# Kernel optimization log

Hardware: AMD Instinct MI355X
Metric: run time of the kernel (lower is better)

The kernel has to match this reference:

```python
import jax, jax.numpy as jnp
import numpy as np

E = 512
H = 8
DH = E // H
LN_EPS = 1e-5


def setup_inputs() -> dict:
    key = jax.random.key(0)
    ks = jax.random.split(key, 8)
    s = 1.0 / np.sqrt(E)
    return {
        "query": jax.random.normal(ks[0], (2, 2048, E), jnp.float32),
        "key_value": jax.random.normal(ks[1], (2, 4096, E), jnp.float32),
        "Wq": jax.random.normal(ks[2], (E, E), jnp.float32) * s,
        "bq": jnp.zeros((E,), jnp.float32),
        "Wk": jax.random.normal(ks[3], (E, E), jnp.float32) * s,
        "bk": jnp.zeros((E,), jnp.float32),
        "Wv": jax.random.normal(ks[4], (E, E), jnp.float32) * s,
        "bv": jnp.zeros((E,), jnp.float32),
        "Wo": jax.random.normal(ks[5], (E, E), jnp.float32) * s,
        "bo": jnp.zeros((E,), jnp.float32),
        "ln_gamma": jnp.ones((E,), jnp.float32),
        "ln_beta": jnp.zeros((E,), jnp.float32),
    }


def reference(query, key_value, Wq, bq, Wk, bk, Wv, bv, Wo, bo, ln_gamma, ln_beta):
    B, Lq, _ = query.shape
    Lk = key_value.shape[1]
    # Projections (torch Linear: x @ W.T + b)
    q = (query @ Wq.T + bq).reshape(B, Lq, H, DH)
    k = (key_value @ Wk.T + bk).reshape(B, Lk, H, DH)
    v = (key_value @ Wv.T + bv).reshape(B, Lk, H, DH)
    scale = 1.0 / np.sqrt(DH).astype(np.float32)
    scores = jnp.einsum("bqhd,bkhd->bhqk", q, k) * scale  # [B,H,Lq,Lk]
    attn = jax.nn.softmax(scores, axis=-1)
    ctx = jnp.einsum("bhqk,bkhd->bqhd", attn, v).reshape(B, Lq, E)
    attn_out = ctx @ Wo.T + bo
    # residual + LayerNorm (dropout is identity in eval)
    x = query + attn_out
    mu = jnp.mean(x, axis=-1, keepdims=True)
    var = jnp.mean(jnp.square(x - mu), axis=-1, keepdims=True)
    return (x - mu) * jax.lax.rsqrt(var + LN_EPS) * ln_gamma + ln_beta
```

## Files before the change

### kernel.cpp

```cpp
#include <hip/hip_runtime.h>
#include <hip/hip_bf16.h>

typedef __bf16 bf16;
typedef __bf16 bf16x8 __attribute__((ext_vector_type(8)));
typedef __bf16 bf16x4 __attribute__((ext_vector_type(4)));
typedef float f32x4 __attribute__((ext_vector_type(4)));
typedef float f32x16 __attribute__((ext_vector_type(16)));
typedef unsigned int u32x4 __attribute__((ext_vector_type(4)));

#define MFMA16(a, b, c) __builtin_amdgcn_mfma_f32_16x16x32_bf16((a), (b), (c), 0, 0, 0)
#define MFMA32(a, b, c) __builtin_amdgcn_mfma_f32_32x32x16_bf16((a), (b), (c), 0, 0, 0)

constexpr int LQ = 2048, LK = 4096, E = 512, H = 8, DH = 64;
#define QSCALE 0.1803368801111137f

#if __has_builtin(__builtin_amdgcn_exp2f)
#define EXP2(x) __builtin_amdgcn_exp2f(x)
#else
#define EXP2(x) __expf(0.6931471805599453f * (x))
#endif

__device__ __forceinline__ bf16x8 ld8(const bf16* p) { return *(const bf16x8*)p; }

__global__ __launch_bounds__(256) void cvt4_kernel(
    const float* __restrict__ w0, const float* __restrict__ w1,
    const float* __restrict__ w2, const float* __restrict__ w3,
    bf16* __restrict__ dst) {
  const float* srcs[4] = {w0, w1, w2, w3};
  const float* src = srcs[blockIdx.y];
  bf16* d = dst + (size_t)blockIdx.y * 262144;
  int i = (blockIdx.x * 256 + threadIdx.x) * 4;
  f32x4 v = *(const f32x4*)(src + i);
  bf16x4 o;
  for (int j = 0; j < 4; ++j) o[j] = (bf16)v[j];
  *(bf16x4*)(d + i) = o;
}

__global__ __launch_bounds__(256) void proj_gemm_kernel(
    const float* __restrict__ query, const float* __restrict__ kv,
    const bf16* __restrict__ Wall,
    const float* __restrict__ bq, const float* __restrict__ bk,
    const float* __restrict__ bv,
    bf16* __restrict__ qproj, bf16* __restrict__ kproj, bf16* __restrict__ vt) {
  __shared__ bf16 smA[2][128][72];
  __shared__ bf16 smB[2][128][72];
  const int tid = threadIdx.x;
  const int lane = tid & 63, wave = tid >> 6;
  const int lrow = lane & 15, quad = lane >> 4;
  const int wm = wave & 1, wn = wave >> 1;

  int x = blockIdx.x, z, mt;
  if (x < 32) { z = 0; mt = x; }
  else if (x < 96) { z = 1; mt = x - 32; }
  else { z = 2; mt = x - 96; }
  const float* A = ((z == 0) ? query : kv) + (size_t)mt * 128 * E;
  const bf16* W = Wall + (size_t)z * 262144;
  const float* bias = (z == 0) ? bq : (z == 1) ? bk : bv;
  const int n0 = blockIdx.y * 128;

  const int arow = tid >> 4, acol = tid & 15;
  const int brow = tid >> 3, bcol = tid & 7;

  f32x4 pa[8];
  bf16x8 pb[4];
#define LOAD_T(t)                                                             \
  {                                                                           \
    for (int p = 0; p < 8; ++p)                                               \
      pa[p] = *(const f32x4*)(A + (size_t)(p * 16 + arow) * E + (t) * 64 +    \
                              acol * 4);                                      \
    for (int p = 0; p < 4; ++p)                                               \
      pb[p] = ld8(W + (size_t)(n0 + p * 32 + brow) * E + (t) * 64 + bcol * 8);\
  }
#define STORE_T(bs)                                                           \
  {                                                                           \
    for (int p = 0; p < 8; ++p) {                                             \
      bf16x4 av;                                                              \
      for (int e = 0; e < 4; ++e) av[e] = (bf16)pa[p][e];                     \
      *(bf16x4*)&smA[bs][p * 16 + arow][acol * 4] = av;                       \
    }                                                                         \
    for (int p = 0; p < 4; ++p)                                               \
      *(bf16x8*)&smB[bs][p * 32 + brow][bcol * 8] = pb[p];                    \
  }

  LOAD_T(0);
  STORE_T(0);
  LOAD_T(1);
  __syncthreads();

  f32x4 acc[4][4] = {};
  for (int t = 0; t < 8; ++t) {
    const int bs = t & 1;
    bf16x8 af[2][4], bfr[2][4];
    for (int ks = 0; ks < 2; ++ks)
      for (int i = 0; i < 4; ++i)
        af[ks][i] = ld8(&smA[bs][wm * 64 + 16 * i + lrow][ks * 32 + quad * 8]);
    for (int ks = 0; ks < 2; ++ks)
      for (int c = 0; c < 4; ++c)
        bfr[ks][c] = ld8(&smB[bs][wn * 64 + 16 * c + lrow][ks * 32 + quad * 8]);
    for (int ks = 0; ks < 2; ++ks)
      for (int i = 0; i < 4; ++i)
        for (int c = 0; c < 4; ++c)
          acc[i][c] = MFMA16(af[ks][i], bfr[ks][c], acc[i][c]);
    if (t < 7) {
      STORE_T(bs ^ 1);
      if (t < 6) LOAD_T(t + 2);
    }
    __syncthreads();
  }
#undef LOAD_T
#undef STORE_T

  const float qsc = (z == 0) ? QSCALE : 1.f;
  float bvl[4];
  for (int c = 0; c < 4; ++c) bvl[c] = bias[n0 + wn * 64 + 16 * c + lrow];
  bf16* Cs = &smA[0][0][0];
  for (int i = 0; i < 4; ++i)
    for (int c = 0; c < 4; ++c)
      for (int r = 0; r < 4; ++r) {
        int row = wm * 64 + 16 * i + 4 * quad + r;
        int col = wn * 64 + 16 * c + lrow;
        bf16 val = (bf16)((acc[i][c][r] + bvl[c]) * qsc);
        if (z < 2) Cs[row * 136 + col] = val;
        else       Cs[col * 136 + row] = val;
      }
  __syncthreads();
  const int rr = tid >> 1, hh = tid & 1;
  if (z == 0) {
    bf16* dstp = qproj + (size_t)(mt * 128 + rr) * E + n0 + hh * 64;
    for (int j = 0; j < 8; ++j)
      *(bf16x8*)(dstp + j * 8) = *(bf16x8*)&Cs[rr * 136 + hh * 64 + j * 8];
  } else if (z == 1) {
    int mtg = mt * 128 + rr;
    int b2 = mtg >> 12, kk = mtg & 4095;
    int t32 = kk >> 5, l31 = kk & 31;
    int bh2 = b2 * 8 + (n0 >> 6) + hh;
    bf16* dstp = kproj + (size_t)bh2 * 262144 + (size_t)t32 * 2048 + l31 * 8;
    for (int j = 0; j < 8; ++j)
      *(bf16x8*)(dstp + j * 256) = *(bf16x8*)&Cs[rr * 136 + hh * 64 + j * 8];
  } else {
    int m0g = mt * 128, b2 = m0g >> 12, kk0 = m0g & 4095;
    int ng = n0 + rr, hd = ng >> 6, d = ng & 63;
    int bh2 = b2 * 8 + hd, dt = d >> 5, l31 = d & 31;
    bf16* dstp = vt + (size_t)bh2 * 262144 + dt * 1024 + l31 * 8;
    for (int j = 0; j < 8; ++j) {
      int kk = kk0 + hh * 64 + 8 * j;
      int t32 = kk >> 5, s = (kk >> 4) & 1, hi2 = (kk >> 3) & 1;
      *(bf16x8*)(dstp + (size_t)t32 * 2048 + s * 512 + hi2 * 256) =
          *(bf16x8*)&Cs[rr * 136 + hh * 64 + j * 8];
    }
  }
}

__global__ __launch_bounds__(256, 2) void attn_kernel(
    const bf16* __restrict__ qp, const bf16* __restrict__ kfg,
    const bf16* __restrict__ vfg, bf16* __restrict__ ctx) {
  const int tid = threadIdx.x;
  const int lane = tid & 63, wave = tid >> 6;
  const int l31 = lane & 31, hi = lane >> 5;
  const int hw = blockIdx.x;
  const int xcd = hw & 7, ii = hw >> 3;
  const int bh = xcd * 2 + (ii >> 5), qt = ii & 31;
  const int b = bh >> 3, h = bh & 7;
  const int q0 = qt * 64;

  __shared__ __align__(16) char smem[34816];

  bf16x8 qf[2][4];
  for (int t = 0; t < 2; ++t)
    for (int st = 0; st < 4; ++st)
      qf[t][st] = ld8(qp + (size_t)(b * LQ + q0 + 32 * t + l31) * E + h * DH +
                      st * 16 + hi * 8);

  float lp[2] = {0.f, 0.f};
  f32x16 acc[2][2] = {};

  const size_t tb = ((size_t)bh * 128 + wave * 32) * 2048;
  const bf16* kb = kfg + tb + hi * 256 + l31 * 8;
  const bf16* vb = vfg + tb + hi * 256 + l31 * 8;

#define LOADT(kf_, vf_, it)                                          \
  {                                                                  \
    const bf16* kp_ = kb + (size_t)(it) * 2048;                      \
    kf_[0] = ld8(kp_);                                               \
    kf_[1] = ld8(kp_ + 512);                                         \
    kf_[2] = ld8(kp_ + 1024);                                        \
    kf_[3] = ld8(kp_ + 1536);                                        \
    const bf16* vp_ = vb + (size_t)(it) * 2048;                      \
    vf_[0] = ld8(vp_);                                               \
    vf_[1] = ld8(vp_ + 512);                                         \
    vf_[2] = ld8(vp_ + 1024);                                        \
    vf_[3] = ld8(vp_ + 1536);                                        \
  }

#define COMPUTE(kf_, vf_)                                            \
  _Pragma("unroll")                                                  \
  for (int t = 0; t < 2; ++t) {                                      \
    f32x16 s_ = {};                                                  \
    __builtin_amdgcn_s_setprio(1);                                   \
    s_ = MFMA32(kf_[0], qf[t][0], s_);                               \
    s_ = MFMA32(kf_[1], qf[t][1], s_);                               \
    s_ = MFMA32(kf_[2], qf[t][2], s_);                               \
    s_ = MFMA32(kf_[3], qf[t][3], s_);                               \
    __builtin_amdgcn_s_setprio(0);                                   \
    unsigned w_[4][2];                                               \
    _Pragma("unroll")                                                \
    for (int t4 = 0; t4 < 4; ++t4)                                   \
      _Pragma("unroll")                                              \
      for (int u = 0; u < 2; ++u) {                                  \
        float e0 = EXP2(s_[4 * t4 + 2 * u]);                         \
        float e1 = EXP2(s_[4 * t4 + 2 * u + 1]);                     \
        lp[t] += e0;                                                 \
        lp[t] += e1;                                                 \
        asm("v_cvt_pk_bf16_f32 %0, %1, %2"                           \
            : "=v"(w_[t4][u])                                        \
            : "v"(e0), "v"(e1));                                     \
      }                                                              \
    bf16x8 paf[2];                                                   \
    _Pragma("unroll")                                                \
    for (int s = 0; s < 2; ++s) {                                    \
      unsigned a0 = w_[2 * s][0], b0 = w_[2 * s + 1][0];             \
      unsigned a1 = w_[2 * s][1], b1 = w_[2 * s + 1][1];             \
      asm("v_permlane32_swap_b32 %0, %1" : "+v"(a0), "+v"(b0));      \
      asm("v_permlane32_swap_b32 %0, %1" : "+v"(a1), "+v"(b1));      \
      u32x4 pw_ = {a0, a1, b0, b1};                                  \
      paf[s] = *(bf16x8*)&pw_;                                       \
    }                                                                \
    __builtin_amdgcn_s_setprio(1);                                   \
    acc[t][0] = MFMA32(paf[0], vf_[0], acc[t][0]);                   \
    acc[t][0] = MFMA32(paf[1], vf_[1], acc[t][0]);                   \
    acc[t][1] = MFMA32(paf[0], vf_[2], acc[t][1]);                   \
    acc[t][1] = MFMA32(paf[1], vf_[3], acc[t][1]);                   \
    __builtin_amdgcn_s_setprio(0);                                   \
  }

  bf16x8 kfA[4], vfA[4], kfB[4], vfB[4];
  LOADT(kfA, vfA, 0);
  for (int it = 0; it < 32; it += 2) {
    LOADT(kfB, vfB, it + 1);
    COMPUTE(kfA, vfA);
    if (it + 2 < 32) LOADT(kfA, vfA, it + 2);
    COMPUTE(kfB, vfB);
  }
#undef LOADT
#undef COMPUTE

  for (int t = 0; t < 2; ++t) lp[t] += __shfl_xor(lp[t], 32);

  float* F = (float*)smem;
  float* Lr = (float*)(smem + 33792);
  if (hi == 0) {
    Lr[wave * 64 + l31] = lp[0];
    Lr[wave * 64 + 32 + l31] = lp[1];
  }
#pragma unroll
  for (int t = 0; t < 2; ++t)
#pragma unroll
    for (int r = 0; r < 16; ++r) {
      int q = 32 * t + (r & 3) + 8 * (r >> 2) + 4 * hi;
      F[(wave * 64 + q) * 33 + l31] = acc[t][0][r];
    }
  __syncthreads();
  const int mq = tid >> 2, d0 = (tid & 3) * 8;
  float ls = Lr[mq] + Lr[64 + mq] + Lr[128 + mq] + Lr[192 + mq];
  const float inv = 1.f / ls;
  {
    float o[8] = {};
#pragma unroll
    for (int w2 = 0; w2 < 4; ++w2) {
      const float* Fr = &F[(w2 * 64 + mq) * 33 + d0];
      for (int j = 0; j < 8; ++j) o[j] += Fr[j];
    }
    bf16x8 ov;
    for (int j = 0; j < 8; ++j) ov[j] = (bf16)(o[j] * inv);
    *(bf16x8*)(ctx + (size_t)(b * LQ + q0 + mq) * E + h * DH + d0) = ov;
  }
  __syncthreads();
#pragma unroll
  for (int t = 0; t < 2; ++t)
#pragma unroll
    for (int r = 0; r < 16; ++r) {
      int q = 32 * t + (r & 3) + 8 * (r >> 2) + 4 * hi;
      F[(wave * 64 + q) * 33 + l31] = acc[t][1][r];
    }
  __syncthreads();
  {
    float o[8] = {};
#pragma unroll
    for (int w2 = 0; w2 < 4; ++w2) {
      const float* Fr = &F[(w2 * 64 + mq) * 33 + d0];
      for (int j = 0; j < 8; ++j) o[j] += Fr[j];
    }
    bf16x8 ov;
    for (int j = 0; j < 8; ++j) ov[j] = (bf16)(o[j] * inv);
    *(bf16x8*)(ctx + (size_t)(b * LQ + q0 + mq) * E + h * DH + 32 + d0) = ov;
  }
}

__global__ __launch_bounds__(512) void outln_kernel(
    const bf16* __restrict__ Cx, const bf16* __restrict__ Wo,
    const float* __restrict__ bo, const float* __restrict__ resid,
    const float* __restrict__ gamma, const float* __restrict__ beta,
    float* __restrict__ out) {
  const int tid = threadIdx.x;
  const int lane = tid & 63, wave = tid >> 6;
  const int lrow = lane & 15, quad = lane >> 4;
  const int m0 = blockIdx.x * 16;
  const int n0 = wave * 64;

  __shared__ bf16 As[16][520];
  __shared__ bf16 Wos[512][72];
  __shared__ float red1[16][8], red2[16][8];
  {
    int r = tid >> 5, ch = tid & 31;
    const bf16* src = Cx + (size_t)(m0 + r) * E + ch * 16;
    *(bf16x8*)&As[r][ch * 16] = ld8(src);
    *(bf16x8*)&As[r][ch * 16 + 8] = ld8(src + 8);
  }
  const int wr = tid >> 3, wc = tid & 7;
  bf16x8 pw[8];
  for (int p = 0; p < 8; ++p)
    pw[p] = ld8(Wo + (size_t)(p * 64 + wr) * E + wc * 8);
  __syncthreads();

  f32x4 acc[4] = {};
  for (int t = 0; t < 8; ++t) {
    for (int p = 0; p < 8; ++p)
      *(bf16x8*)&Wos[p * 64 + wr][wc * 8] = pw[p];
    __syncthreads();
    if (t < 7)
      for (int p = 0; p < 8; ++p)
        pw[p] = ld8(Wo + (size_t)(p * 64 + wr) * E + (t + 1) * 64 + wc * 8);
    for (int ks = 0; ks < 2; ++ks) {
      bf16x8 a = *(const bf16x8*)&As[lrow][t * 64 + ks * 32 + quad * 8];
      for (int c = 0; c < 4; ++c) {
        bf16x8 w = *(const bf16x8*)&Wos[n0 + 16 * c + lrow][ks * 32 + quad * 8];
        acc[c] = MFMA16(a, w, acc[c]);
      }
    }
    __syncthreads();
  }

  float s1[4] = {}, s2[4] = {};
  for (int c = 0; c < 4; ++c) {
    int n = n0 + 16 * c + lrow;
    float bb = bo[n];
    for (int r = 0; r < 4; ++r) {
      int m = 4 * quad + r;
      float xv = acc[c][r] + bb + resid[(size_t)(m0 + m) * E + n];
      acc[c][r] = xv;
      s1[r] += xv;
      s2[r] += xv * xv;
    }
  }
  for (int off = 1; off < 16; off <<= 1)
    for (int r = 0; r < 4; ++r) {
      s1[r] += __shfl_xor(s1[r], off);
      s2[r] += __shfl_xor(s2[r], off);
    }
  if (lrow == 0)
    for (int r = 0; r < 4; ++r) {
      red1[4 * quad + r][wave] = s1[r];
      red2[4 * quad + r][wave] = s2[r];
    }
  __syncthreads();
  float mu[4], rstd[4];
  for (int r = 0; r < 4; ++r) {
    int m = 4 * quad + r;
    float t1 = 0.f, t2 = 0.f;
    for (int w = 0; w < 8; ++w) { t1 += red1[m][w]; t2 += red2[m][w]; }
    float mean = t1 * (1.f / 512.f);
    float var = t2 * (1.f / 512.f) - mean * mean;
    mu[r] = mean;
    rstd[r] = rsqrtf(var + 1e-5f);
  }
  for (int c = 0; c < 4; ++c) {
    int n = n0 + 16 * c + lrow;
    float gm = gamma[n], bt = beta[n];
    for (int r = 0; r < 4; ++r) {
      int m = m0 + 4 * quad + r;
      out[(size_t)m * E + n] = (acc[c][r] - mu[r]) * rstd[r] * gm + bt;
    }
  }
}

extern "C" void kernel_launch(void* const* d_in, const int* in_sizes, int n_in,
                              void* d_out, int out_size, void* d_ws, size_t ws_size,
                              hipStream_t stream) {
  const float* query     = (const float*)d_in[0];
  const float* key_value = (const float*)d_in[1];
  const float* Wq = (const float*)d_in[2];
  const float* bq = (const float*)d_in[3];
  const float* Wk = (const float*)d_in[4];
  const float* bk = (const float*)d_in[5];
  const float* Wv = (const float*)d_in[6];
  const float* bv = (const float*)d_in[7];
  const float* Wo = (const float*)d_in[8];
  const float* bo = (const float*)d_in[9];
  const float* gamma = (const float*)d_in[10];
  const float* beta  = (const float*)d_in[11];
  float* out = (float*)d_out;

  bf16* Wb    = (bf16*)d_ws;
  bf16* Wob   = Wb + (size_t)3 * 262144;
  bf16* qproj = Wb + (size_t)4 * 262144;
  bf16* kproj = qproj + (size_t)4096 * 512;
  bf16* vt    = kproj + (size_t)8192 * 512;

  cvt4_kernel<<<dim3(256, 4), 256, 0, stream>>>(Wq, Wk, Wv, Wo, Wb);
  proj_gemm_kernel<<<dim3(160, 4), 256, 0, stream>>>(
      query, key_value, Wb, bq, bk, bv, qproj, kproj, vt);
  attn_kernel<<<512, 256, 0, stream>>>(qproj, kproj, vt, qproj );
  outln_kernel<<<256, 512, 0, stream>>>(qproj, Wob, bo, query, gamma, beta, out);
}
```

Before: 165.4 us.

## Split out-projection+LayerNorm into tiled GEMM and separate LayerNorm kernel

Replaces the fused out-projection/LayerNorm kernel, which used 16-row blocks and reloaded all of Wo per block, with a 128x128-tiled double-buffered MFMA GEMM that writes fp32 results to workspace. A separate row-wise LayerNorm kernel then adds bias and residual and normalizes. This cuts redundant Wo traffic and improves MFMA reuse, at the cost of an extra launch and an fp32 intermediate round trip through memory.

After: 163.7 us. Within noise of the previous version (-1.1%).

```diff
diff --git a/kernel.cpp b/kernel.cpp
--- a/kernel.cpp
+++ b/kernel.cpp
@@ -296,91 +296,117 @@
   }
 }
 
-__global__ __launch_bounds__(512) void outln_kernel(
+__global__ __launch_bounds__(256) void outgemm_kernel(
     const bf16* __restrict__ Cx, const bf16* __restrict__ Wo,
-    const float* __restrict__ bo, const float* __restrict__ resid,
-    const float* __restrict__ gamma, const float* __restrict__ beta,
-    float* __restrict__ out) {
+    float* __restrict__ y) {
+  __shared__ bf16 smA[2][128][72];
+  __shared__ bf16 smB[2][128][72];
   const int tid = threadIdx.x;
   const int lane = tid & 63, wave = tid >> 6;
   const int lrow = lane & 15, quad = lane >> 4;
-  const int m0 = blockIdx.x * 16;
-  const int n0 = wave * 64;
-
-  __shared__ bf16 As[16][520];
-  __shared__ bf16 Wos[512][72];
-  __shared__ float red1[16][8], red2[16][8];
-  {
-    int r = tid >> 5, ch = tid & 31;
-    const bf16* src = Cx + (size_t)(m0 + r) * E + ch * 16;
-    *(bf16x8*)&As[r][ch * 16] = ld8(src);
-    *(bf16x8*)&As[r][ch * 16 + 8] = ld8(src + 8);
-  }
-  const int wr = tid >> 3, wc = tid & 7;
-  bf16x8 pw[8];
-  for (int p = 0; p < 8; ++p)
-    pw[p] = ld8(Wo + (size_t)(p * 64 + wr) * E + wc * 8);
-  __syncthreads();
-
-  f32x4 acc[4] = {};
+  const int wm = wave & 1, wn = wave >> 1;
+  const int m0 = blockIdx.x * 128, n0 = blockIdx.y * 128;
+  const bf16* A = Cx + (size_t)m0 * E;
+
+  const int srow = tid >> 3, schunk = tid & 7;
+
+  bf16x8 pa[4], pb[4];
+#define LOAD_T(t)                                                             \
+  {                                                                           \
+    for (int p = 0; p < 4; ++p)                                               \
+      pa[p] = ld8(A + (size_t)(p * 32 + srow) * E + (t) * 64 + schunk * 8);   \
+    for (int p = 0; p < 4; ++p)                                               \
+      pb[p] = ld8(Wo + (size_t)(n0 + p * 32 + srow) * E + (t) * 64 +          \
+                  schunk * 8);                                                \
+  }
+#define STORE_T(bs)                                                           \
+  {                                                                           \
+    for (int p = 0; p < 4; ++p)                                               \
+      *(bf16x8*)&smA[bs][p * 32 + srow][schunk * 8] = pa[p];                  \
+    for (int p = 0; p < 4; ++p)                                               \
+      *(bf16x8*)&smB[bs][p * 32 + srow][schunk * 8] = pb[p];                  \
+  }
+
+  LOAD_T(0);
+  STORE_T(0);
+  LOAD_T(1);
+  __syncthreads();
+
+  f32x4 acc[4][4] = {};
   for (int t = 0; t < 8; ++t) {
-    for (int p = 0; p < 8; ++p)
-      *(bf16x8*)&Wos[p * 64 + wr][wc * 8] = pw[p];
+    const int bs = t & 1;
+    bf16x8 af[2][4], bfr[2][4];
+    for (int ks = 0; ks < 2; ++ks)
+      for (int i = 0; i < 4; ++i)
+        af[ks][i] = ld8(&smA[bs][wm * 64 + 16 * i + lrow][ks * 32 + quad * 8]);
+    for (int ks = 0; ks < 2; ++ks)
+      for (int c = 0; c < 4; ++c)
+        bfr[ks][c] = ld8(&smB[bs][wn * 64 + 16 * c + lrow][ks * 32 + quad * 8]);
+    for (int ks = 0; ks < 2; ++ks)
+      for (int i = 0; i < 4; ++i)
+        for (int c = 0; c < 4; ++c)
+          acc[i][c] = MFMA16(af[ks][i], bfr[ks][c], acc[i][c]);
+    if (t < 7) {
+      STORE_T(bs ^ 1);
+      if (t < 6) LOAD_T(t + 2);
+    }
     __syncthreads();
-    if (t < 7)
-      for (int p = 0; p < 8; ++p)
-        pw[p] = ld8(Wo + (size_t)(p * 64 + wr) * E + (t + 1) * 64 + wc * 8);
-    for (int ks = 0; ks < 2; ++ks) {
-      bf16x8 a = *(const bf16x8*)&As[lrow][t * 64 + ks * 32 + quad * 8];
-      for (int c = 0; c < 4; ++c) {
-        bf16x8 w = *(const bf16x8*)&Wos[n0 + 16 * c + lrow][ks * 32 + quad * 8];
-        acc[c] = MFMA16(a, w, acc[c]);
+  }
+#undef LOAD_T
+#undef STORE_T
+
+  for (int i = 0; i < 4; ++i)
+    for (int c = 0; c < 4; ++c)
+      for (int r = 0; r < 4; ++r) {
+        int row = m0 + wm * 64 + 16 * i + 4 * quad + r;
+        int col = n0 + wn * 64 + 16 * c + lrow;
+        y[(size_t)row * E + col] = acc[i][c][r];
       }
-    }
-    __syncthreads();
-  }
-
-  float s1[4] = {}, s2[4] = {};
-  for (int c = 0; c < 4; ++c) {
-    int n = n0 + 16 * c + lrow;
-    float bb = bo[n];
-    for (int r = 0; r < 4; ++r) {
-      int m = 4 * quad + r;
-      float xv = acc[c][r] + bb + resid[(size_t)(m0 + m) * E + n];
-      acc[c][r] = xv;
-      s1[r] += xv;
-      s2[r] += xv * xv;
-    }
-  }
-  for (int off = 1; off < 16; off <<= 1)
-    for (int r = 0; r < 4; ++r) {
-      s1[r] += __shfl_xor(s1[r], off);
-      s2[r] += __shfl_xor(s2[r], off);
-    }
-  if (lrow == 0)
-    for (int r = 0; r < 4; ++r) {
-      red1[4 * quad + r][wave] = s1[r];
-      red2[4 * quad + r][wave] = s2[r];
-    }
-  __syncthreads();
-  float mu[4], rstd[4];
-  for (int r = 0; r < 4; ++r) {
-    int m = 4 * quad + r;
-    float t1 = 0.f, t2 = 0.f;
-    for (int w = 0; w < 8; ++w) { t1 += red1[m][w]; t2 += red2[m][w]; }
-    float mean = t1 * (1.f / 512.f);
-    float var = t2 * (1.f / 512.f) - mean * mean;
-    mu[r] = mean;
-    rstd[r] = rsqrtf(var + 1e-5f);
-  }
-  for (int c = 0; c < 4; ++c) {
-    int n = n0 + 16 * c + lrow;
-    float gm = gamma[n], bt = beta[n];
-    for (int r = 0; r < 4; ++r) {
-      int m = m0 + 4 * quad + r;
-      out[(size_t)m * E + n] = (acc[c][r] - mu[r]) * rstd[r] * gm + bt;
-    }
-  }
+}
+
+__global__ __launch_bounds__(256) void ln_kernel(
+    const float* __restrict__ y, const float* __restrict__ resid,
+    const float* __restrict__ bo, const float* __restrict__ gamma,
+    const float* __restrict__ beta, float* __restrict__ out) {
+  const int tid = threadIdx.x;
+  const int lane = tid & 63, wave = tid >> 6;
+  const int row = blockIdx.x * 4 + wave;
+  const int c0 = lane * 8;
+
+  const float* yr = y + (size_t)row * E + c0;
+  const float* rr = resid + (size_t)row * E + c0;
+  f32x4 y0 = *(const f32x4*)yr, y1 = *(const f32x4*)(yr + 4);
+  f32x4 r0 = *(const f32x4*)rr, r1 = *(const f32x4*)(rr + 4);
+  f32x4 b0 = *(const f32x4*)(bo + c0), b1 = *(const f32x4*)(bo + c0 + 4);
+
+  float xv[8];
+  float s1 = 0.f, s2 = 0.f;
+  for (int j = 0; j < 4; ++j) {
+    xv[j] = y0[j] + r0[j] + b0[j];
+    xv[4 + j] = y1[j] + r1[j] + b1[j];
+  }
+  for (int j = 0; j < 8; ++j) {
+    s1 += xv[j];
+    s2 += xv[j] * xv[j];
+  }
+  for (int off = 1; off < 64; off <<= 1) {
+    s1 += __shfl_xor(s1, off);
+    s2 += __shfl_xor(s2, off);
+  }
+  const float mean = s1 * (1.f / 512.f);
+  const float var = s2 * (1.f / 512.f) - mean * mean;
+  const float rstd = rsqrtf(var + 1e-5f);
+
+  f32x4 g0 = *(const f32x4*)(gamma + c0), g1 = *(const f32x4*)(gamma + c0 + 4);
+  f32x4 t0 = *(const f32x4*)(beta + c0), t1 = *(const f32x4*)(beta + c0 + 4);
+  f32x4 o0, o1;
+  for (int j = 0; j < 4; ++j) {
+    o0[j] = (xv[j] - mean) * rstd * g0[j] + t0[j];
+    o1[j] = (xv[4 + j] - mean) * rstd * g1[j] + t1[j];
+  }
+  float* op = out + (size_t)row * E + c0;
+  *(f32x4*)op = o0;
+  *(f32x4*)(op + 4) = o1;
 }
 
 extern "C" void kernel_launch(void* const* d_in, const int* in_sizes, int n_in,
@@ -405,10 +431,12 @@
   bf16* qproj = Wb + (size_t)4 * 262144;
   bf16* kproj = qproj + (size_t)4096 * 512;
   bf16* vt    = kproj + (size_t)8192 * 512;
+  float* y    = (float*)(vt + (size_t)8192 * 512);
 
   cvt4_kernel<<<dim3(256, 4), 256, 0, stream>>>(Wq, Wk, Wv, Wo, Wb);
   proj_gemm_kernel<<<dim3(160, 4), 256, 0, stream>>>(
       query, key_value, Wb, bq, bk, bv, qproj, kproj, vt);
   attn_kernel<<<512, 256, 0, stream>>>(qproj, kproj, vt, qproj );
-  outln_kernel<<<256, 512, 0, stream>>>(qproj, Wob, bo, query, gamma, beta, out);
-}
+  outgemm_kernel<<<dim3(32, 4), 256, 0, stream>>>(qproj, Wob, y);
+  ln_kernel<<<1024, 256, 0, stream>>>(y, query, bo, gamma, beta, out);
+}
```
